# Optimization experiments

Hardware: AMD Instinct MI355X
Metric: run time of the kernel (lower is better)

Reference implementation:

```python
import jax, jax.numpy as jnp
import numpy as np

N = 100000      # nodes
E = 1600000     # edges
F_IN = 512      # num_node_features
HID = 128       # hidden_dim (GCN2Conv channels)
C = 64          # num_classes
L = 8           # n_layers
ALPHA = 0.1
THETA = 0.5


def setup_inputs() -> dict:
    key = jax.random.key(0)
    ks = jax.random.split(key, 7)
    x = jax.random.normal(ks[0], (N, F_IN), jnp.float32)
    edge_index = jax.random.randint(ks[1], (2, E), 0, N, dtype=jnp.int64)
    # fcs[0]: Linear(F_IN, HID); stored as [in, out] so forward is x @ w + b
    w_in = jax.random.normal(ks[2], (F_IN, HID), jnp.float32) / np.sqrt(F_IN)
    b_in = jnp.zeros((HID,), jnp.float32)
    # one shared [H, H] weight per GCN2Conv layer (shared_weights=True)
    conv_w = jax.random.normal(ks[3], (L, HID, HID), jnp.float32) / np.sqrt(HID)
    # fcs[-1]: Linear(HID, C)
    w_out = jax.random.normal(ks[4], (HID, C), jnp.float32) / np.sqrt(HID)
    b_out = jnp.zeros((C,), jnp.float32)
    return dict(x=x, edge_index=edge_index, w_in=w_in, b_in=b_in,
                conv_w=conv_w, w_out=w_out, b_out=b_out)


def _gcn_norm(edge_index, num_nodes):
    # PyG gcn_norm with add_self_loops=True, edge_weight=1
    loops = jnp.arange(num_nodes, dtype=edge_index.dtype)
    src = jnp.concatenate([edge_index[0], loops])
    dst = jnp.concatenate([edge_index[1], loops])
    deg = jax.ops.segment_sum(jnp.ones_like(dst, jnp.float32), dst,
                              num_segments=num_nodes)
    dinv = jnp.where(deg > 0, jax.lax.rsqrt(jnp.maximum(deg, 1e-12)), 0.0)
    norm = dinv[src] * dinv[dst]  # [E + N]
    return src, dst, norm


def reference(x, edge_index, w_in, b_in, conv_w, w_out, b_out):
    src, dst, norm = _gcn_norm(edge_index, N)
    h = x @ w_in + b_in          # fcs[0]; [N, HID]
    h0 = h                       # initial residual
    for l in range(L):
        beta = float(np.log(THETA / (l + 1) + 1.0))
        # sparse neighbor aggregation: out[i] = sum_e norm[e] * h[src[e]]
        agg = jax.ops.segment_sum(h[src] * norm[:, None], dst, num_segments=N)
        s = (1.0 - ALPHA) * agg + ALPHA * h0           # initial residual mix
        h = jax.nn.elu((1.0 - beta) * s + beta * (s @ conv_w[l]))  # identity mapping
        # dropout omitted (eval mode / training=False)
    logits = h @ w_out + b_out   # fcs[-1]
    return jax.nn.log_softmax(logits, axis=-1)
```

## Files before the change

kernel.cpp:

```cpp
#include <hip/hip_runtime.h>
#include <math.h>

#define N_NODES 100000
#define N_EDGES 1600000
#define F_IN    512
#define HID     128
#define NCLS    64
#define NLAYERS 8
#define NT      (N_NODES / 16)
#define NSCANB  ((N_NODES + 255) / 256)

typedef __attribute__((ext_vector_type(8))) short short8;
typedef __attribute__((ext_vector_type(4))) float float4v;

#define SWZB(b) ((b) ^ ((((b) >> 8) & 3) << 4))

__device__ inline unsigned short f2bf(float f) {
    unsigned int u = __float_as_uint(f);
    unsigned int r = u + 0x7fffu + ((u >> 16) & 1u);
    return (unsigned short)(r >> 16);
}
__device__ inline float bf2f(unsigned short h) {
    return __uint_as_float(((unsigned int)h) << 16);
}
__device__ inline uint4 pack8(const unsigned short* v) {
    uint4 u;
    u.x = (unsigned)v[0] | ((unsigned)v[1] << 16);
    u.y = (unsigned)v[2] | ((unsigned)v[3] << 16);
    u.z = (unsigned)v[4] | ((unsigned)v[5] << 16);
    u.w = (unsigned)v[6] | ((unsigned)v[7] << 16);
    return u;
}
__device__ inline void bf8_fma(float* a, uint4 u, float v) {
    a[0] += v * __uint_as_float(u.x << 16);
    a[1] += v * __uint_as_float(u.x & 0xffff0000u);
    a[2] += v * __uint_as_float(u.y << 16);
    a[3] += v * __uint_as_float(u.y & 0xffff0000u);
    a[4] += v * __uint_as_float(u.z << 16);
    a[5] += v * __uint_as_float(u.z & 0xffff0000u);
    a[6] += v * __uint_as_float(u.w << 16);
    a[7] += v * __uint_as_float(u.w & 0xffff0000u);
}
__device__ inline void unpack8(float* f, uint4 u) {
    f[0] = __uint_as_float(u.x << 16); f[1] = __uint_as_float(u.x & 0xffff0000u);
    f[2] = __uint_as_float(u.y << 16); f[3] = __uint_as_float(u.y & 0xffff0000u);
    f[4] = __uint_as_float(u.z << 16); f[5] = __uint_as_float(u.z & 0xffff0000u);
    f[6] = __uint_as_float(u.w << 16); f[7] = __uint_as_float(u.w & 0xffff0000u);
}
__device__ inline void split_into(short8& ahi, short8& alo, int j, float f) {
    unsigned short h = f2bf(f);
    ahi[j] = (short)h;
    alo[j] = (short)f2bf(f - bf2f(h));
}


__global__ __launch_bounds__(256) void cnt_init(int* __restrict__ cnt) {
    int i = blockIdx.x * 256 + threadIdx.x;
    if (i < N_NODES) cnt[i] = 0;
}
__global__ __launch_bounds__(256) void cnt_count(const int* __restrict__ dst,
                                                 int* __restrict__ cnt) {
    int e = blockIdx.x * 256 + threadIdx.x;
    if (e < N_EDGES) atomicAdd(&cnt[dst[e]], 1);
}
__global__ __launch_bounds__(256) void make_dinv(const int* __restrict__ cnt,
                                                 float* __restrict__ dinv) {
    int i = blockIdx.x * 256 + threadIdx.x;
    if (i < N_NODES) dinv[i] = rsqrtf((float)(cnt[i] + 1));
}
__global__ __launch_bounds__(256) void scan_block(const int* __restrict__ cnt,
                                                  int* __restrict__ partial,
                                                  int* __restrict__ bsum) {
    __shared__ int tmp[256];
    int t = threadIdx.x, i = blockIdx.x * 256 + t;
    int v = (i < N_NODES) ? cnt[i] : 0;
    tmp[t] = v;
    __syncthreads();
#pragma unroll
    for (int off = 1; off < 256; off <<= 1) {
        int add = (t >= off) ? tmp[t - off] : 0;
        __syncthreads();
        tmp[t] += add;
        __syncthreads();
    }
    if (i < N_NODES) partial[i] = tmp[t];
    if (t == 255) bsum[blockIdx.x] = tmp[255];
}
__global__ void scan_bsum(int* __restrict__ bsum) {
    if (threadIdx.x == 0 && blockIdx.x == 0) {
        int acc = 0;
        for (int i = 0; i < NSCANB; i++) { int v = bsum[i]; bsum[i] = acc; acc += v; }
    }
}
__global__ __launch_bounds__(256) void finalize_rowptr(const int* __restrict__ cnt,
                                                       const int* __restrict__ partial,
                                                       const int* __restrict__ bsum,
                                                       int* __restrict__ row_ptr,
                                                       int* __restrict__ cursor) {
    int i = blockIdx.x * 256 + threadIdx.x;
    if (i < N_NODES) {
        int ex = partial[i] - cnt[i] + bsum[blockIdx.x];
        row_ptr[i] = ex;
        cursor[i]  = ex;
        if (i == N_NODES - 1) row_ptr[N_NODES] = ex + cnt[i];
    }
}
__global__ __launch_bounds__(256) void scatter_edges(const int* __restrict__ srcI,
                                                     const int* __restrict__ dstI,
                                                     const float* __restrict__ dinv,
                                                     int* __restrict__ cursor,
                                                     int2* __restrict__ rec) {
    int e = blockIdx.x * 256 + threadIdx.x;
    if (e < N_EDGES) {
        int s = srcI[e], d = dstI[e];
        int pos = atomicAdd(&cursor[d], 1);
        rec[pos] = make_int2(s, __float_as_int(dinv[s] * dinv[d]));
    }
}

__global__ __launch_bounds__(64) void conv_win(const float* __restrict__ w,
                                               unsigned short* __restrict__ wip) {
    int nt = blockIdx.x >> 4;
    int c  = blockIdx.x & 15;
    int lane = threadIdx.x;
    int n  = nt * 16 + (lane & 15);
    int kb = c * 32 + (lane >> 4) * 8;
    unsigned short hi[8], lo[8];
#pragma unroll
    for (int j = 0; j < 8; j++) {
        float v = w[(size_t)(kb + j) * HID + n];
        hi[j] = f2bf(v);
        lo[j] = f2bf(v - bf2f(hi[j]));
    }
    size_t base = ((size_t)c * 8 + nt) * 1024 + (size_t)lane * 8;
    *(uint4*)&wip[base]       = pack8(hi);
    *(uint4*)&wip[base + 512] = pack8(lo);
}

__global__ __launch_bounds__(64) void conv_wl(const float* __restrict__ cw,
                                              unsigned short* __restrict__ wlp) {
    int l  = blockIdx.x >> 5;
    int nt = (blockIdx.x >> 2) & 7;
    int c  = blockIdx.x & 3;
    int lane = threadIdx.x;
    float beta = logf(0.5f / (float)(l + 1) + 1.0f);
    int n  = nt * 16 + (lane & 15);
    int kb = c * 32 + (lane >> 4) * 8;
    const float* W = cw + (size_t)l * HID * HID;
    unsigned short hi[8], lo[8];
#pragma unroll
    for (int j = 0; j < 8; j++) {
        int k = kb + j;
        float v = beta * W[(size_t)k * HID + n] + ((k == n) ? (1.0f - beta) : 0.0f);
        hi[j] = f2bf(v);
        lo[j] = f2bf(v - bf2f(hi[j]));
    }
    size_t base = (size_t)l * 32768 + ((size_t)c * 8 + nt) * 1024 + (size_t)lane * 8;
    *(uint4*)&wlp[base]       = pack8(hi);
    *(uint4*)&wlp[base + 512] = pack8(lo);
}

__global__ __launch_bounds__(64) void conv_wout(const float* __restrict__ w,
                                                unsigned short* __restrict__ wop) {
    int nt = blockIdx.x >> 2;
    int c  = blockIdx.x & 3;
    int lane = threadIdx.x;
    int n  = nt * 16 + (lane & 15);
    int kb = c * 32 + (lane >> 4) * 8;
    unsigned short hi[8], lo[8];
#pragma unroll
    for (int j = 0; j < 8; j++) {
        float v = w[(size_t)(kb + j) * NCLS + n];
        hi[j] = f2bf(v);
        lo[j] = f2bf(v - bf2f(hi[j]));
    }
    size_t base = ((size_t)nt * 4 + c) * 1024 + (size_t)lane * 8;
    *(uint4*)&wop[base]       = pack8(hi);
    *(uint4*)&wop[base + 512] = pack8(lo);
}

__global__ __launch_bounds__(256) void in_gemm_mfma(const float* __restrict__ x,
        const unsigned short* __restrict__ wip, const float* __restrict__ bias,
        unsigned short* __restrict__ hb, unsigned short* __restrict__ h0b) {
    __shared__ unsigned short wlds[8192];
    __shared__ unsigned short tile[64][136];
    int tid = threadIdx.x;
    int wave = tid >> 6, lane = tid & 63;
    int t = blockIdx.x * 4 + wave;
    int m = lane & 15, q = lane >> 4;
    int tc = (t < NT) ? t : (NT - 1);

    const uint4* wg = (const uint4*)wip;
    uint4 pf0 = wg[tid];
    uint4 pf1 = wg[tid + 256];
    uint4 pf2 = wg[tid + 512];
    uint4 pf3 = wg[tid + 768];

    float4v acc[8];
#pragma unroll
    for (int nt = 0; nt < 8; nt++) acc[nt] = (float4v){0.f, 0.f, 0.f, 0.f};
    const float* xr = x + (size_t)(tc * 16 + m) * F_IN + q * 8;
    uint4* wl4 = (uint4*)wlds;

    for (int c = 0; c < 16; c++) {
        wl4[tid] = pf0; wl4[tid + 256] = pf1; wl4[tid + 512] = pf2; wl4[tid + 768] = pf3;
        __syncthreads();
        if (c < 15) {
            const uint4* wn = wg + (size_t)(c + 1) * 1024;
            pf0 = wn[tid]; pf1 = wn[tid + 256]; pf2 = wn[tid + 512]; pf3 = wn[tid + 768];
        }
        float4 x0 = *(const float4*)(xr + c * 32);
        float4 x1 = *(const float4*)(xr + c * 32 + 4);
        short8 ahi, alo;
        split_into(ahi, alo, 0, x0.x); split_into(ahi, alo, 1, x0.y);
        split_into(ahi, alo, 2, x0.z); split_into(ahi, alo, 3, x0.w);
        split_into(ahi, alo, 4, x1.x); split_into(ahi, alo, 5, x1.y);
        split_into(ahi, alo, 6, x1.z); split_into(ahi, alo, 7, x1.w);
#pragma unroll
        for (int nt = 0; nt < 8; nt++) {
            short8 bhi = *(short8*)&wlds[nt * 1024 + lane * 8];
            short8 blo = *(short8*)&wlds[nt * 1024 + 512 + lane * 8];
            acc[nt] = __builtin_amdgcn_mfma_f32_16x16x32_bf16(ahi, bhi, acc[nt], 0, 0, 0);
            acc[nt] = __builtin_amdgcn_mfma_f32_16x16x32_bf16(ahi, blo, acc[nt], 0, 0, 0);
            acc[nt] = __builtin_amdgcn_mfma_f32_16x16x32_bf16(alo, bhi, acc[nt], 0, 0, 0);
        }
        __syncthreads();
    }

    if (t < NT) {
#pragma unroll
        for (int nt = 0; nt < 8; nt++) {
            float bb = bias[nt * 16 + m];
#pragma unroll
            for (int r = 0; r < 4; r++)
                tile[wave * 16 + q * 4 + r][nt * 16 + m] = f2bf(acc[nt][r] + bb);
        }
    }
    __syncthreads();

    int nl = tid >> 2, part = tid & 3;
    int node = blockIdx.x * 64 + nl;
    if (node < N_NODES) {
        uint4* d1 = (uint4*)&hb [(size_t)node * HID + part * 32];
        uint4* d2 = (uint4*)&h0b[(size_t)node * HID + part * 32];
#pragma unroll
        for (int j = 0; j < 4; j++) {
            uint4 u = *(uint4*)&tile[nl][part * 32 + j * 8];
            d1[j] = u; d2[j] = u;
        }
    }
}

template <int LAST>
__global__ __launch_bounds__(256, 4) void spmm_gemm(const int* __restrict__ row_ptr,
        const int2* __restrict__ rec, const float* __restrict__ dinv,
        const unsigned short* __restrict__ hin, const unsigned short* __restrict__ h0b,
        const unsigned short* __restrict__ wlp, void* __restrict__ outp) {
    __shared__ __align__(16) unsigned short afr[16384];
    int tid = threadIdx.x;
    int wave = tid >> 6, lane = tid & 63;
    int qu = lane >> 4, fl = lane & 15;
    char* af = (char*)afr;

    int base = blockIdx.x * 64 + wave * 16;
#pragma unroll 1
    for (int g = 0; g < 4; ++g) {
        int node = base + g * 4 + qu;
        int nc = (node < N_NODES) ? node : (N_NODES - 1);
        int e0 = row_ptr[nc], e1 = row_ptr[nc + 1];
        float a[8] = {0.f, 0.f, 0.f, 0.f, 0.f, 0.f, 0.f, 0.f};
        int e = e0;
        for (; e + 3 < e1; e += 4) {
            int2 r0 = rec[e], r1 = rec[e + 1], r2 = rec[e + 2], r3 = rec[e + 3];
            uint4 u0 = *(const uint4*)(hin + (size_t)r0.x * HID + fl * 8);
            uint4 u1 = *(const uint4*)(hin + (size_t)r1.x * HID + fl * 8);
            uint4 u2 = *(const uint4*)(hin + (size_t)r2.x * HID + fl * 8);
            uint4 u3 = *(const uint4*)(hin + (size_t)r3.x * HID + fl * 8);
            bf8_fma(a, u0, __int_as_float(r0.y));
            bf8_fma(a, u1, __int_as_float(r1.y));
            bf8_fma(a, u2, __int_as_float(r2.y));
            bf8_fma(a, u3, __int_as_float(r3.y));
        }
        for (; e < e1; ++e) {
            int2 r0 = rec[e];
            uint4 u0 = *(const uint4*)(hin + (size_t)r0.x * HID + fl * 8);
            bf8_fma(a, u0, __int_as_float(r0.y));
        }
        float dd = dinv[nc], d2 = dd * dd;
        float hvf[8], zvf[8];
        unpack8(hvf, *(const uint4*)(hin + (size_t)nc * HID + fl * 8));
        unpack8(zvf, *(const uint4*)(h0b + (size_t)nc * HID + fl * 8));
        short8 ohi, olo;
#pragma unroll
        for (int j = 0; j < 8; ++j) {
            float o = 0.9f * (a[j] + d2 * hvf[j]) + 0.1f * zvf[j];
            split_into(ohi, olo, j, o);
        }
        int mrow = g * 4 + qu;
        int b0 = wave * 8192 + (fl >> 2) * 2048 + (fl & 3) * 256 + mrow * 16;
        *(short8*)(af + SWZB(b0)) = ohi;
        *(short8*)(af + SWZB(b0 + 1024)) = olo;
    }
    __syncthreads();

    float4v acc[8];
#pragma unroll
    for (int nt = 0; nt < 8; ++nt) acc[nt] = (float4v){0.f, 0.f, 0.f, 0.f};
    const short8* wp8 = (const short8*)wlp;
#pragma unroll
    for (int c = 0; c < 4; ++c) {
        int rb = wave * 8192 + c * 2048 + lane * 16;
        short8 ahi = *(const short8*)(af + SWZB(rb));
        short8 alo = *(const short8*)(af + SWZB(rb + 1024));
#pragma unroll
        for (int nt = 0; nt < 8; ++nt) {
            short8 bhi = wp8[(size_t)(c * 8 + nt) * 128 + lane];
            short8 blo = wp8[(size_t)(c * 8 + nt) * 128 + 64 + lane];
            acc[nt] = __builtin_amdgcn_mfma_f32_16x16x32_bf16(ahi, bhi, acc[nt], 0, 0, 0);
            acc[nt] = __builtin_amdgcn_mfma_f32_16x16x32_bf16(ahi, blo, acc[nt], 0, 0, 0);
            acc[nt] = __builtin_amdgcn_mfma_f32_16x16x32_bf16(alo, bhi, acc[nt], 0, 0, 0);
        }
    }

    if (LAST) {
        int t = blockIdx.x * 4 + wave;
        if (t < NT) {
            float* hf = (float*)outp;
#pragma unroll
            for (int nt = 0; nt < 8; ++nt) {
#pragma unroll
                for (int r = 0; r < 4; ++r) {
                    float v = acc[nt][r];
                    v = (v > 0.f) ? v : (expf(v) - 1.0f);
                    hf[(size_t)(t * 16 + qu * 4 + r) * HID + nt * 16 + fl] = v;
                }
            }
        }
    } else {
        __syncthreads();
        unsigned short (*tile)[136] = (unsigned short (*)[136])afr;
#pragma unroll
        for (int nt = 0; nt < 8; ++nt) {
#pragma unroll
            for (int r = 0; r < 4; ++r) {
                float v = acc[nt][r];
                v = (v > 0.f) ? v : (expf(v) - 1.0f);
                tile[wave * 16 + qu * 4 + r][nt * 16 + fl] = f2bf(v);
            }
        }
        __syncthreads();
        unsigned short* hout = (unsigned short*)outp;
        int nl = tid >> 2, part = tid & 3;
        int node = blockIdx.x * 64 + nl;
        if (node < N_NODES) {
            uint4* d1 = (uint4*)&hout[(size_t)node * HID + part * 32];
#pragma unroll
            for (int j = 0; j < 4; ++j) d1[j] = *(uint4*)&tile[nl][part * 32 + j * 8];
        }
    }
}

__global__ __launch_bounds__(256) void out_gemm(const float* __restrict__ hf,
        const unsigned short* __restrict__ wop, const float* __restrict__ bias,
        float* __restrict__ out) {
    int wave = threadIdx.x >> 6;
    int lane = threadIdx.x & 63;
    int t = blockIdx.x * 4 + wave;
    int m = lane & 15, q = lane >> 4;
    if (t >= NT) return;

    float4v acc[4];
#pragma unroll
    for (int nt = 0; nt < 4; nt++) acc[nt] = (float4v){0.f, 0.f, 0.f, 0.f};
    const float* hr = hf + (size_t)(t * 16 + m) * HID + q * 8;
    const short8* wp8 = (const short8*)wop;
#pragma unroll
    for (int c = 0; c < 4; c++) {
        float4 x0 = *(const float4*)(hr + c * 32);
        float4 x1 = *(const float4*)(hr + c * 32 + 4);
        short8 ahi, alo;
        split_into(ahi, alo, 0, x0.x); split_into(ahi, alo, 1, x0.y);
        split_into(ahi, alo, 2, x0.z); split_into(ahi, alo, 3, x0.w);
        split_into(ahi, alo, 4, x1.x); split_into(ahi, alo, 5, x1.y);
        split_into(ahi, alo, 6, x1.z); split_into(ahi, alo, 7, x1.w);
#pragma unroll
        for (int nt = 0; nt < 4; nt++) {
            short8 bhi = wp8[(size_t)(nt * 4 + c) * 128 + lane];
            short8 blo = wp8[(size_t)(nt * 4 + c) * 128 + 64 + lane];
            acc[nt] = __builtin_amdgcn_mfma_f32_16x16x32_bf16(ahi, bhi, acc[nt], 0, 0, 0);
            acc[nt] = __builtin_amdgcn_mfma_f32_16x16x32_bf16(ahi, blo, acc[nt], 0, 0, 0);
            acc[nt] = __builtin_amdgcn_mfma_f32_16x16x32_bf16(alo, bhi, acc[nt], 0, 0, 0);
        }
    }
    float bn[4];
#pragma unroll
    for (int nt = 0; nt < 4; nt++) bn[nt] = bias[nt * 16 + m];
#pragma unroll
    for (int r = 0; r < 4; r++) {
        float v0 = acc[0][r] + bn[0], v1 = acc[1][r] + bn[1];
        float v2 = acc[2][r] + bn[2], v3 = acc[3][r] + bn[3];
        float mx = fmaxf(fmaxf(v0, v1), fmaxf(v2, v3));
#pragma unroll
        for (int msk = 1; msk < 16; msk <<= 1) mx = fmaxf(mx, __shfl_xor(mx, msk));
        float ssum = expf(v0 - mx) + expf(v1 - mx) + expf(v2 - mx) + expf(v3 - mx);
#pragma unroll
        for (int msk = 1; msk < 16; msk <<= 1) ssum += __shfl_xor(ssum, msk);
        float lg = mx + logf(ssum);
        size_t base = (size_t)(t * 16 + q * 4 + r) * NCLS + m;
        out[base]      = v0 - lg;
        out[base + 16] = v1 - lg;
        out[base + 32] = v2 - lg;
        out[base + 48] = v3 - lg;
    }
}


extern "C" void kernel_launch(void* const* d_in, const int* in_sizes, int n_in,
                              void* d_out, int out_size, void* d_ws, size_t ws_size,
                              hipStream_t stream) {
    const float* x      = (const float*)d_in[0];
    const int*   ei     = (const int*)  d_in[1];
    const float* w_in   = (const float*)d_in[2];
    const float* b_in   = (const float*)d_in[3];
    const float* conv_w = (const float*)d_in[4];
    const float* w_out  = (const float*)d_in[5];
    const float* b_out  = (const float*)d_in[6];
    float* out = (float*)d_out;

    const int* srcI = ei;
    const int* dstI = ei + N_EDGES;

    char* ws = (char*)d_ws;
    float* dinv    = (float*)(ws + 0x000000);
    int*   cnt     = (int*)  (ws + 0x080000);
    int*   partial = (int*)  (ws + 0x100000);
    int*   bsum    = (int*)  (ws + 0x180000);
    int*   row_ptr = (int*)  (ws + 0x190000);
    int*   cursor  = (int*)  (ws + 0x200000);
    int2*  rec     = (int2*) (ws + 0x280000);
    unsigned short* wip = (unsigned short*)(ws + 0xF00000);
    unsigned short* wlp = (unsigned short*)(ws + 0xF40000);
    unsigned short* wop = (unsigned short*)(ws + 0xFC0000);
    unsigned short* hb  = (unsigned short*)(ws + 0x1000000);
    unsigned short* h0b = hb + (size_t)N_NODES * HID;
    unsigned short* hb2 = h0b + (size_t)N_NODES * HID;
    float* hf = (float*)(hb2 + 2 * (size_t)N_NODES * HID);

    int gN = (N_NODES + 255) / 256;
    int gE = (N_EDGES + 255) / 256;
    int gT = (NT + 3) / 4;

    cnt_init<<<gN, 256, 0, stream>>>(cnt);
    cnt_count<<<gE, 256, 0, stream>>>(dstI, cnt);
    make_dinv<<<gN, 256, 0, stream>>>(cnt, dinv);
    scan_block<<<NSCANB, 256, 0, stream>>>(cnt, partial, bsum);
    scan_bsum<<<1, 64, 0, stream>>>(bsum);
    finalize_rowptr<<<NSCANB, 256, 0, stream>>>(cnt, partial, bsum, row_ptr, cursor);
    scatter_edges<<<gE, 256, 0, stream>>>(srcI, dstI, dinv, cursor, rec);

    conv_win<<<128, 64, 0, stream>>>(w_in, wip);
    conv_wl<<<256, 64, 0, stream>>>(conv_w, wlp);
    conv_wout<<<16, 64, 0, stream>>>(w_out, wop);

    in_gemm_mfma<<<gT, 256, 0, stream>>>(x, wip, b_in, hb, h0b);

    unsigned short* cur = hb;
    unsigned short* nxt = hb2;
    for (int l = 0; l < NLAYERS; l++) {
        const unsigned short* wl = wlp + (size_t)l * 32768;
        if (l < NLAYERS - 1) {
            spmm_gemm<0><<<gT, 256, 0, stream>>>(row_ptr, rec, dinv, cur, h0b, wl, nxt);
            unsigned short* t = cur; cur = nxt; nxt = t;
        } else {
            spmm_gemm<1><<<gT, 256, 0, stream>>>(row_ptr, rec, dinv, cur, h0b, wl, hf);
        }
    }

    out_gemm<<<gT, 256, 0, stream>>>(hf, wop, b_out, out);
}
```

Baseline: 1.218 ms.

## Bucket CSR edges by source-node chunk to improve gather locality

Builds the CSR with 8 sub-buckets per destination keyed by which eighth of the source-node range the edge comes from, using a two-level scan over 800k counters. The SpMM then walks the buckets in order, so all waves gather source rows from roughly the same region of h at the same time, which is meant to improve L2/MALL hit rates on the random gathers. It also hoists the self and h0 row loads ahead of the edge loop. The costs are a larger preprocessing pass (8x counters, extra scan kernels), shuffles for the bucket bounds, and a shorter unroll (2 instead of 4) inside each bucket.

```diff
diff --git a/kernel.cpp b/kernel.cpp
--- a/kernel.cpp
+++ b/kernel.cpp
@@ -8,7 +8,11 @@
 #define NCLS    64
 #define NLAYERS 8
 #define NT      (N_NODES / 16)
-#define NSCANB  ((N_NODES + 255) / 256)
+#define NCHUNK  8
+#define CHSZ    (N_NODES / NCHUNK)
+#define N8      (N_NODES * NCHUNK)
+#define G8      (N8 / 256)
+#define G8B     ((G8 + 255) / 256)
 
 typedef __attribute__((ext_vector_type(8))) short short8;
 typedef __attribute__((ext_vector_type(4))) float float4v;
@@ -54,66 +58,73 @@
 }
 
 
-__global__ __launch_bounds__(256) void cnt_init(int* __restrict__ cnt) {
+__global__ __launch_bounds__(256) void zero16(int* __restrict__ cnt16) {
     int i = blockIdx.x * 256 + threadIdx.x;
-    if (i < N_NODES) cnt[i] = 0;
-}
-__global__ __launch_bounds__(256) void cnt_count(const int* __restrict__ dst,
-                                                 int* __restrict__ cnt) {
-    int e = blockIdx.x * 256 + threadIdx.x;
-    if (e < N_EDGES) atomicAdd(&cnt[dst[e]], 1);
-}
-__global__ __launch_bounds__(256) void make_dinv(const int* __restrict__ cnt,
-                                                 float* __restrict__ dinv) {
-    int i = blockIdx.x * 256 + threadIdx.x;
-    if (i < N_NODES) dinv[i] = rsqrtf((float)(cnt[i] + 1));
-}
-__global__ __launch_bounds__(256) void scan_block(const int* __restrict__ cnt,
-                                                  int* __restrict__ partial,
-                                                  int* __restrict__ bsum) {
-    __shared__ int tmp[256];
-    int t = threadIdx.x, i = blockIdx.x * 256 + t;
-    int v = (i < N_NODES) ? cnt[i] : 0;
-    tmp[t] = v;
-    __syncthreads();
-#pragma unroll
-    for (int off = 1; off < 256; off <<= 1) {
-        int add = (t >= off) ? tmp[t - off] : 0;
-        __syncthreads();
-        tmp[t] += add;
-        __syncthreads();
-    }
-    if (i < N_NODES) partial[i] = tmp[t];
-    if (t == 255) bsum[blockIdx.x] = tmp[255];
-}
-__global__ void scan_bsum(int* __restrict__ bsum) {
-    if (threadIdx.x == 0 && blockIdx.x == 0) {
-        int acc = 0;
-        for (int i = 0; i < NSCANB; i++) { int v = bsum[i]; bsum[i] = acc; acc += v; }
-    }
-}
-__global__ __launch_bounds__(256) void finalize_rowptr(const int* __restrict__ cnt,
-                                                       const int* __restrict__ partial,
-                                                       const int* __restrict__ bsum,
-                                                       int* __restrict__ row_ptr,
-                                                       int* __restrict__ cursor) {
-    int i = blockIdx.x * 256 + threadIdx.x;
-    if (i < N_NODES) {
-        int ex = partial[i] - cnt[i] + bsum[blockIdx.x];
-        row_ptr[i] = ex;
-        cursor[i]  = ex;
-        if (i == N_NODES - 1) row_ptr[N_NODES] = ex + cnt[i];
-    }
-}
-__global__ __launch_bounds__(256) void scatter_edges(const int* __restrict__ srcI,
-                                                     const int* __restrict__ dstI,
-                                                     const float* __restrict__ dinv,
-                                                     int* __restrict__ cursor,
-                                                     int2* __restrict__ rec) {
+    if (i < N8) cnt16[i] = 0;
+}
+__global__ __launch_bounds__(256) void cnt16_count(const int* __restrict__ srcI,
+                                                   const int* __restrict__ dstI,
+                                                   int* __restrict__ cnt16) {
     int e = blockIdx.x * 256 + threadIdx.x;
     if (e < N_EDGES) {
         int s = srcI[e], d = dstI[e];
-        int pos = atomicAdd(&cursor[d], 1);
+        atomicAdd(&cnt16[d * NCHUNK + s / CHSZ], 1);
+    }
+}
+__global__ __launch_bounds__(256) void scan_incl(const int* __restrict__ in, int n,
+                                                 int* __restrict__ part,
+                                                 int* __restrict__ bsum) {
+    __shared__ int tmp[256];
+    int t = threadIdx.x, i = blockIdx.x * 256 + t;
+    int v = (i < n) ? in[i] : 0;
+    tmp[t] = v;
+    __syncthreads();
+#pragma unroll
+    for (int off = 1; off < 256; off <<= 1) {
+        int add = (t >= off) ? tmp[t - off] : 0;
+        __syncthreads();
+        tmp[t] += add;
+        __syncthreads();
+    }
+    if (i < n) part[i] = tmp[t];
+    if (t == 255) bsum[blockIdx.x] = tmp[255];
+}
+__global__ void scan_ser(int* __restrict__ b, int n) {
+    if (threadIdx.x == 0 && blockIdx.x == 0) {
+        int acc = 0;
+        for (int i = 0; i < n; i++) { int v = b[i]; b[i] = acc; acc += v; }
+    }
+}
+__global__ __launch_bounds__(256) void finalize16(const int* __restrict__ cnt16,
+        const int* __restrict__ part1, const int* __restrict__ part2,
+        const int* __restrict__ b1, const int* __restrict__ b2,
+        int* __restrict__ ptr16, int* __restrict__ cursor16) {
+    int i = blockIdx.x * 256 + threadIdx.x;
+    if (i < N8) {
+        int j = i >> 8;
+        int ex = part1[i] - cnt16[i] + (part2[j] - b1[j]) + b2[j >> 8];
+        ptr16[i] = ex;
+        cursor16[i] = ex;
+        if (i == N8 - 1) ptr16[N8] = ex + cnt16[i];
+    }
+}
+__global__ __launch_bounds__(256) void make_dinv16(const int* __restrict__ ptr16,
+                                                   float* __restrict__ dinv) {
+    int i = blockIdx.x * 256 + threadIdx.x;
+    if (i < N_NODES) {
+        int deg = ptr16[i * NCHUNK + NCHUNK] - ptr16[i * NCHUNK];
+        dinv[i] = rsqrtf((float)(deg + 1));
+    }
+}
+__global__ __launch_bounds__(256) void scatter16(const int* __restrict__ srcI,
+                                                 const int* __restrict__ dstI,
+                                                 const float* __restrict__ dinv,
+                                                 int* __restrict__ cursor16,
+                                                 int2* __restrict__ rec) {
+    int e = blockIdx.x * 256 + threadIdx.x;
+    if (e < N_EDGES) {
+        int s = srcI[e], d = dstI[e];
+        int pos = atomicAdd(&cursor16[d * NCHUNK + s / CHSZ], 1);
         rec[pos] = make_int2(s, __float_as_int(dinv[s] * dinv[d]));
     }
 }
@@ -252,7 +263,7 @@
 }
 
 template <int LAST>
-__global__ __launch_bounds__(256, 4) void spmm_gemm(const int* __restrict__ row_ptr,
+__global__ __launch_bounds__(256, 4) void spmm_gemm(const int* __restrict__ ptr16,
         const int2* __restrict__ rec, const float* __restrict__ dinv,
         const unsigned short* __restrict__ hin, const unsigned short* __restrict__ h0b,
         const unsigned short* __restrict__ wlp, void* __restrict__ outp) {
@@ -267,29 +278,32 @@
     for (int g = 0; g < 4; ++g) {
         int node = base + g * 4 + qu;
         int nc = (node < N_NODES) ? node : (N_NODES - 1);
-        int e0 = row_ptr[nc], e1 = row_ptr[nc + 1];
+        int pv = ptr16[nc * NCHUNK + ((fl < 9) ? fl : 8)];
+        float dd = dinv[nc];
+        uint4 hv = *(const uint4*)(hin + (size_t)nc * HID + fl * 8);
+        uint4 zv = *(const uint4*)(h0b + (size_t)nc * HID + fl * 8);
         float a[8] = {0.f, 0.f, 0.f, 0.f, 0.f, 0.f, 0.f, 0.f};
-        int e = e0;
-        for (; e + 3 < e1; e += 4) {
-            int2 r0 = rec[e], r1 = rec[e + 1], r2 = rec[e + 2], r3 = rec[e + 3];
-            uint4 u0 = *(const uint4*)(hin + (size_t)r0.x * HID + fl * 8);
-            uint4 u1 = *(const uint4*)(hin + (size_t)r1.x * HID + fl * 8);
-            uint4 u2 = *(const uint4*)(hin + (size_t)r2.x * HID + fl * 8);
-            uint4 u3 = *(const uint4*)(hin + (size_t)r3.x * HID + fl * 8);
-            bf8_fma(a, u0, __int_as_float(r0.y));
-            bf8_fma(a, u1, __int_as_float(r1.y));
-            bf8_fma(a, u2, __int_as_float(r2.y));
-            bf8_fma(a, u3, __int_as_float(r3.y));
-        }
-        for (; e < e1; ++e) {
-            int2 r0 = rec[e];
-            uint4 u0 = *(const uint4*)(hin + (size_t)r0.x * HID + fl * 8);
-            bf8_fma(a, u0, __int_as_float(r0.y));
-        }
-        float dd = dinv[nc], d2 = dd * dd;
+        for (int c = 0; c < NCHUNK; ++c) {
+            int e0 = __shfl(pv, (qu << 4) + c);
+            int e1 = __shfl(pv, (qu << 4) + c + 1);
+            int e = e0;
+            for (; e + 1 < e1; e += 2) {
+                int2 r0 = rec[e], r1 = rec[e + 1];
+                uint4 u0 = *(const uint4*)(hin + (size_t)r0.x * HID + fl * 8);
+                uint4 u1 = *(const uint4*)(hin + (size_t)r1.x * HID + fl * 8);
+                bf8_fma(a, u0, __int_as_float(r0.y));
+                bf8_fma(a, u1, __int_as_float(r1.y));
+            }
+            if (e < e1) {
+                int2 r0 = rec[e];
+                uint4 u0 = *(const uint4*)(hin + (size_t)r0.x * HID + fl * 8);
+                bf8_fma(a, u0, __int_as_float(r0.y));
+            }
+        }
+        float d2 = dd * dd;
         float hvf[8], zvf[8];
-        unpack8(hvf, *(const uint4*)(hin + (size_t)nc * HID + fl * 8));
-        unpack8(zvf, *(const uint4*)(h0b + (size_t)nc * HID + fl * 8));
+        unpack8(hvf, hv);
+        unpack8(zvf, zv);
         short8 ohi, olo;
 #pragma unroll
         for (int j = 0; j < 8; ++j) {
@@ -432,11 +446,6 @@
 
     char* ws = (char*)d_ws;
     float* dinv    = (float*)(ws + 0x000000);
-    int*   cnt     = (int*)  (ws + 0x080000);
-    int*   partial = (int*)  (ws + 0x100000);
-    int*   bsum    = (int*)  (ws + 0x180000);
-    int*   row_ptr = (int*)  (ws + 0x190000);
-    int*   cursor  = (int*)  (ws + 0x200000);
     int2*  rec     = (int2*) (ws + 0x280000);
     unsigned short* wip = (unsigned short*)(ws + 0xF00000);
     unsigned short* wlp = (unsigned short*)(ws + 0xF40000);
@@ -445,18 +454,26 @@
     unsigned short* h0b = hb + (size_t)N_NODES * HID;
     unsigned short* hb2 = h0b + (size_t)N_NODES * HID;
     float* hf = (float*)(hb2 + 2 * (size_t)N_NODES * HID);
+    int* ptr16    = (int*)(hf + (size_t)N_NODES * HID);
+    int* cursor16 = ptr16 + (N8 + 64);
+    int* cnt16    = cursor16 + N8;
+    int* part1    = cnt16 + N8;
+    int* b1       = part1 + N8;
+    int* part2    = b1 + 4096;
+    int* b2       = part2 + 4096;
 
     int gN = (N_NODES + 255) / 256;
     int gE = (N_EDGES + 255) / 256;
     int gT = (NT + 3) / 4;
 
-    cnt_init<<<gN, 256, 0, stream>>>(cnt);
-    cnt_count<<<gE, 256, 0, stream>>>(dstI, cnt);
-    make_dinv<<<gN, 256, 0, stream>>>(cnt, dinv);
-    scan_block<<<NSCANB, 256, 0, stream>>>(cnt, partial, bsum);
-    scan_bsum<<<1, 64, 0, stream>>>(bsum);
-    finalize_rowptr<<<NSCANB, 256, 0, stream>>>(cnt, partial, bsum, row_ptr, cursor);
-    scatter_edges<<<gE, 256, 0, stream>>>(srcI, dstI, dinv, cursor, rec);
+    zero16<<<G8, 256, 0, stream>>>(cnt16);
+    cnt16_count<<<gE, 256, 0, stream>>>(srcI, dstI, cnt16);
+    scan_incl<<<G8, 256, 0, stream>>>(cnt16, N8, part1, b1);
+    scan_incl<<<G8B, 256, 0, stream>>>(b1, G8, part2, b2);
+    scan_ser<<<1, 64, 0, stream>>>(b2, G8B);
+    finalize16<<<G8, 256, 0, stream>>>(cnt16, part1, part2, b1, b2, ptr16, cursor16);
+    make_dinv16<<<gN, 256, 0, stream>>>(ptr16, dinv);
+    scatter16<<<gE, 256, 0, stream>>>(srcI, dstI, dinv, cursor16, rec);
 
     conv_win<<<128, 64, 0, stream>>>(w_in, wip);
     conv_wl<<<256, 64, 0, stream>>>(conv_w, wlp);
@@ -469,10 +486,10 @@
     for (int l = 0; l < NLAYERS; l++) {
         const unsigned short* wl = wlp + (size_t)l * 32768;
         if (l < NLAYERS - 1) {
-            spmm_gemm<0><<<gT, 256, 0, stream>>>(row_ptr, rec, dinv, cur, h0b, wl, nxt);
+            spmm_gemm<0><<<gT, 256, 0, stream>>>(ptr16, rec, dinv, cur, h0b, wl, nxt);
             unsigned short* t = cur; cur = nxt; nxt = t;
         } else {
-            spmm_gemm<1><<<gT, 256, 0, stream>>>(row_ptr, rec, dinv, cur, h0b, wl, hf);
+            spmm_gemm<1><<<gT, 256, 0, stream>>>(ptr16, rec, dinv, cur, h0b, wl, hf);
         }
     }
 
```

Result: slower. 1.656 ms (+35.9%).
